# Kernel tuning notes

Measured on AMD Instinct MI355X. Metric: run time of the kernel, lower is better.

Reference implementation:

```python
import jax, jax.numpy as jnp
import numpy as np

EMBED_DIM = 512
NUM_HEADS = 8
HEAD_DIM = EMBED_DIM // NUM_HEADS
FACTOR = 5
B, T = 4, 2048


def setup_inputs() -> dict:
    key = jax.random.key(0)
    ks = jax.random.split(key, 10)
    s = EMBED_DIM ** -0.5
    hidden_states = jax.random.normal(ks[0], (B, T, EMBED_DIM), dtype=jnp.float32)
    log_L = int(np.ceil(np.log1p(T)))
    u_part = min(FACTOR * T * log_L, T)
    index_sample = jax.random.randint(ks[1], (u_part,), 0, T, dtype=jnp.int32)
    Wq = jax.random.normal(ks[2], (EMBED_DIM, EMBED_DIM), dtype=jnp.float32) * s
    bq = jnp.zeros((EMBED_DIM,), dtype=jnp.float32)
    Wk = jax.random.normal(ks[3], (EMBED_DIM, EMBED_DIM), dtype=jnp.float32) * s
    bk = jnp.zeros((EMBED_DIM,), dtype=jnp.float32)
    Wv = jax.random.normal(ks[4], (EMBED_DIM, EMBED_DIM), dtype=jnp.float32) * s
    bv = jnp.zeros((EMBED_DIM,), dtype=jnp.float32)
    Wo = jax.random.normal(ks[5], (EMBED_DIM, EMBED_DIM), dtype=jnp.float32) * s
    bo = jnp.zeros((EMBED_DIM,), dtype=jnp.float32)
    return {"hidden_states": hidden_states, "index_sample": index_sample,
            "Wq": Wq, "bq": bq, "Wk": Wk, "bk": bk, "Wv": Wv, "bv": bv,
            "Wo": Wo, "bo": bo}


def _split_heads(x, bsz, seqlen):
    # [B, T, E] -> [B*H, T, head_dim]
    return x.reshape(bsz, seqlen, NUM_HEADS, HEAD_DIM).transpose(0, 2, 1, 3).reshape(bsz * NUM_HEADS, seqlen, HEAD_DIM)


def reference(hidden_states, index_sample, Wq, bq, Wk, bk, Wv, bv, Wo, bo):
    bsz, tgt_len, embed_dim = hidden_states.shape
    scaling = HEAD_DIM ** -0.5
    q = (hidden_states @ Wq.T + bq) * scaling
    k = hidden_states @ Wk.T + bk
    v = hidden_states @ Wv.T + bv
    q = _split_heads(q, bsz, tgt_len)   # [BH, T, d]
    k = _split_heads(k, bsz, tgt_len)
    v = _split_heads(v, bsz, tgt_len)
    L_k = tgt_len
    log_q = int(np.ceil(np.log1p(tgt_len)))
    u = min(FACTOR * log_q, tgt_len)
    # random key sampling (indices precomputed, length u_part)
    k_sample = k[:, index_sample, :]                                  # [BH, u_part, d]
    qk_sample = jnp.einsum('bqd,bkd->bqk', q, k_sample)               # [BH, T, u_part]
    # sparsity measurement: max - mean over sampled keys (mean uses full L_k as in source)
    sparsity = qk_sample.max(axis=-1) - qk_sample.sum(axis=-1) / L_k  # [BH, T]
    top_idx = jax.lax.top_k(sparsity, u)[1]                           # [BH, u]
    q_reduce = jnp.take_along_axis(q, top_idx[:, :, None], axis=1)    # [BH, u, d]
    attn = jax.nn.softmax(jnp.einsum('bud,bkd->buk', q_reduce, k), axis=-1)  # [BH, u, L]
    attn_out = jnp.einsum('buk,bkd->bud', attn, v)                    # [BH, u, d]
    # encoder context: mean of values over time, scattered with active-query outputs
    context = jnp.broadcast_to(v.mean(axis=1, keepdims=True), v.shape)  # [BH, T, d]
    bh_idx = jnp.arange(bsz * NUM_HEADS)[:, None]
    context = context.at[bh_idx, top_idx].set(attn_out)
    out = context.reshape(bsz, NUM_HEADS, tgt_len, HEAD_DIM).transpose(0, 2, 1, 3).reshape(bsz, tgt_len, embed_dim)
    return out @ Wo.T + bo
```

## Files before the change

kernel.cpp:

```cpp
#include <hip/hip_runtime.h>
#include <hip/hip_bf16.h>
#include <math.h>

#define T_LEN 2048
#define EMB   512
#define NHEAD 8
#define HDIM  64
#define BHEADS 32
#define USEL  40

typedef __bf16 bf16v8 __attribute__((ext_vector_type(8)));
typedef _Float16 f16x8 __attribute__((ext_vector_type(8)));
typedef float f32x4 __attribute__((ext_vector_type(4)));
typedef unsigned short u16;

__device__ __forceinline__ void cvt4_hilo(const float4 f, uint2& ph, uint2& pl)
{
    __hip_bfloat16 h0 = __float2bfloat16(f.x);
    __hip_bfloat16 h1 = __float2bfloat16(f.y);
    __hip_bfloat16 h2 = __float2bfloat16(f.z);
    __hip_bfloat16 h3 = __float2bfloat16(f.w);
    __hip_bfloat16 l0 = __float2bfloat16(f.x - __bfloat162float(h0));
    __hip_bfloat16 l1 = __float2bfloat16(f.y - __bfloat162float(h1));
    __hip_bfloat16 l2 = __float2bfloat16(f.z - __bfloat162float(h2));
// ... 493 lines not shown
        else if (w == 1) { gsrc = kp + 4096;  ldst = KH + 4096; }
        else if (w == 2) { gsrc = kp + 8192;  ldst = KL; }
        else             { gsrc = kp + 12288; ldst = KL + 4096; }
        #pragma unroll
        for (int i = 0; i < 8; ++i)
            __builtin_amdgcn_global_load_lds(
                (const __attribute__((address_space(1))) void*)(gsrc + (size_t)lane * 8 + i * 512),
                (__attribute__((address_space(3))) void*)(ldst + i * 512),
                16, 0, 0);
        __syncthreads();

        #pragma unroll
        for (int j = 0; j < 8; ++j) {
            int rb0 = kq * 1024 + (j * 16 + lm) * 8;
            int rb1 = 4096 + kq * 1024 + (j * 16 + lm) * 8;
            f16x8 bh0 = *(const f16x8*)&KH[rb0];
            f16x8 bl0 = *(const f16x8*)&KL[rb0];
            f16x8 bh1 = *(const f16x8*)&KH[rb1];
            f16x8 bl1 = *(const f16x8*)&KL[rb1];
            f32x4 a0 = {0.f, 0.f, 0.f, 0.f};
            f32x4 a1 = {0.f, 0.f, 0.f, 0.f};
            a0 = __builtin_amdgcn_mfma_f32_16x16x32_f16(qh[0][0], bh0, a0, 0, 0, 0);
            a1 = __builtin_amdgcn_mfma_f32_16x16x32_f16(qh[1][0], bh0, a1, 0, 0, 0);
            a0 = __builtin_amdgcn_mfma_f32_16x16x32_f16(qh[0][0], bl0, a0, 0, 0, 0);
            a1 = __builtin_amdgcn_mfma_f32_16x16x32_f16(qh[1][0], bl0, a1, 0, 0, 0);
            a0 = __builtin_amdgcn_mfma_f32_16x16x32_f16(ql[0][0], bh0, a0, 0, 0, 0);
            a1 = __builtin_amdgcn_mfma_f32_16x16x32_f16(ql[1][0], bh0, a1, 0, 0, 0);
            a0 = __builtin_amdgcn_mfma_f32_16x16x32_f16(qh[0][1], bh1, a0, 0, 0, 0);
            a1 = __builtin_amdgcn_mfma_f32_16x16x32_f16(qh[1][1], bh1, a1, 0, 0, 0);
            a0 = __builtin_amdgcn_mfma_f32_16x16x32_f16(qh[0][1], bl1, a0, 0, 0, 0);
            a1 = __builtin_amdgcn_mfma_f32_16x16x32_f16(qh[1][1], bl1, a1, 0, 0, 0);
            a0 = __builtin_amdgcn_mfma_f32_16x16x32_f16(ql[0][1], bh1, a0, 0, 0, 0);
            a1 = __builtin_amdgcn_mfma_f32_16x16x32_f16(ql[1][1], bh1, a1, 0, 0, 0);
            #pragma unroll
            for (int r = 0; r < 4; ++r) {
                vmax[0][r] = fmaxf(vmax[0][r], a0[r]);
                vmax[1][r] = fmaxf(vmax[1][r], a1[r]);
            }
        }
    }

    #pragma unroll
    for (int i = 0; i < 2; ++i)
        #pragma unroll
        for (int r = 0; r < 4; ++r) {
            float m = vmax[i][r];
            m = fmaxf(m, __shfl_xor(m, 1, 64));
            m = fmaxf(m, __shfl_xor(m, 2, 64));
            m = fmaxf(m, __shfl_xor(m, 4, 64));
            m = fmaxf(m, __shfl_xor(m, 8, 64));
            if (lm == 0) smax[w * 32 + i * 16 + kq * 4 + r] = m;
        }
    __syncthreads();

    if (tid < 128)
        spars[bh * T_LEN + q0 + tid] = smax[tid] - sdotL[tid] * (1.0f / 2048.0f);
}

__global__ __launch_bounds__(256)
void sparsity_scan_fb_kernel(const float* __restrict__ q, const float* __restrict__ k,
                             const float* __restrict__ ksum, const int* __restrict__ klist,
                             const int* __restrict__ ncp, float* __restrict__ spars)
{
    alignas(16) __shared__ u16 KH[256 * 40];
    alignas(16) __shared__ u16 KL[256 * 40];
    __shared__ float ksm[64];
    __shared__ float smax[128];
    __shared__ float sdotL[128];

    const int tid = threadIdx.x;
    const int bh = blockIdx.y;
    const int q0 = blockIdx.x * 128;
    const int w = tid >> 6, lane = tid & 63;
    const int lm = lane & 15, kq = lane >> 4;

    const float* qb = q + ((size_t)bh * T_LEN + q0) * HDIM;
    const float4* kb4 = (const float4*)(k + (size_t)bh * T_LEN * HDIM);
    const int ntiles = (ncp[0] + 127) >> 7;

    if (tid < 64) ksm[tid] = ksum[bh * 64 + tid];

    #pragma unroll
    for (int s = 0; s < 8; ++s) {
        int u = tid + 256 * s;
        int row = u >> 4, c4 = u & 15;
        float4 f = *(const float4*)&qb[row * HDIM + c4 * 4];
        uint2 ph, pl;
        cvt4_hilo_h(f, ph, pl);
        int base = ((c4 >> 3) * 128 + row) * 40 + (c4 & 7) * 4;
        *(uint2*)&KH[base] = ph;
        *(uint2*)&KL[base] = pl;
    }
    __syncthreads();

    f16x8 qh[2][2], ql[2][2];
    #pragma unroll
    for (int i = 0; i < 2; ++i)
        #pragma unroll
        for (int c = 0; c < 2; ++c) {
            int ra = (c * 128 + w * 32 + i * 16 + lm) * 40 + kq * 8;
            qh[i][c] = *(const f16x8*)&KH[ra];
            ql[i][c] = *(const f16x8*)&KL[ra];
        }

    {
        float4 k0a = *(const float4*)&ksm[kq * 8];
        float4 k0b = *(const float4*)&ksm[kq * 8 + 4];
        float4 k1a = *(const float4*)&ksm[32 + kq * 8];
        float4 k1b = *(const float4*)&ksm[32 + kq * 8 + 4];
        float kmv[2][8] = {{k0a.x, k0a.y, k0a.z, k0a.w, k0b.x, k0b.y, k0b.z, k0b.w},
                           {k1a.x, k1a.y, k1a.z, k1a.w, k1b.x, k1b.y, k1b.z, k1b.w}};
        #pragma unroll
        for (int i = 0; i < 2; ++i) {
            float sd = 0.f;
            #pragma unroll
            for (int c = 0; c < 2; ++c)
                #pragma unroll
                for (int e = 0; e < 8; ++e)
                    sd = fmaf((float)qh[i][c][e] + (float)ql[i][c][e], kmv[c][e], sd);
            sd += __shfl_xor(sd, 16, 64);
            sd += __shfl_xor(sd, 32, 64);
            if (kq == 0) sdotL[w * 32 + i * 16 + lm] = sd;
        }
    }

    float vmax[2][4];
    #pragma unroll
    for (int i = 0; i < 2; ++i)
        #pragma unroll
        for (int r = 0; r < 4; ++r) vmax[i][r] = -INFINITY;

    for (int kt = 0; kt < ntiles; ++kt) {
        __syncthreads();
        #pragma unroll
        for (int s = 0; s < 8; ++s) {
            int u = tid + 256 * s;
            int row = u >> 4, c4 = u & 15;
            int krow = klist[kt * 128 + row];
            float4 f = kb4[krow * 16 + c4];
            uint2 ph, pl;
            cvt4_hilo_h(f, ph, pl);
            int base = ((c4 >> 3) * 128 + row) * 40 + (c4 & 7) * 4;
            *(uint2*)&KH[base] = ph;
            *(uint2*)&KL[base] = pl;
        }
        __syncthreads();

        #pragma unroll
        for (int j = 0; j < 8; ++j) {
            int rb0 = (j * 16 + lm) * 40 + kq * 8;
            int rb1 = (128 + j * 16 + lm) * 40 + kq * 8;
            f16x8 bh0 = *(const f16x8*)&KH[rb0];
            f16x8 bl0 = *(const f16x8*)&KL[rb0];
            f16x8 bh1 = *(const f16x8*)&KH[rb1];
            f16x8 bl1 = *(const f16x8*)&KL[rb1];
            f32x4 a0 = {0.f, 0.f, 0.f, 0.f};
            f32x4 a1 = {0.f, 0.f, 0.f, 0.f};
            a0 = __builtin_amdgcn_mfma_f32_16x16x32_f16(qh[0][0], bh0, a0, 0, 0, 0);
            a1 = __builtin_amdgcn_mfma_f32_16x16x32_f16(qh[1][0], bh0, a1, 0, 0, 0);
            a0 = __builtin_amdgcn_mfma_f32_16x16x32_f16(qh[0][0], bl0, a0, 0, 0, 0);
            a1 = __builtin_amdgcn_mfma_f32_16x16x32_f16(qh[1][0], bl0, a1, 0, 0, 0);
            a0 = __builtin_amdgcn_mfma_f32_16x16x32_f16(ql[0][0], bh0, a0, 0, 0, 0);
            a1 = __builtin_amdgcn_mfma_f32_16x16x32_f16(ql[1][0], bh0, a1, 0, 0, 0);
            a0 = __builtin_amdgcn_mfma_f32_16x16x32_f16(qh[0][1], bh1, a0, 0, 0, 0);
            a1 = __builtin_amdgcn_mfma_f32_16x16x32_f16(qh[1][1], bh1, a1, 0, 0, 0);
            a0 = __builtin_amdgcn_mfma_f32_16x16x32_f16(qh[0][1], bl1, a0, 0, 0, 0);
            a1 = __builtin_amdgcn_mfma_f32_16x16x32_f16(qh[1][1], bl1, a1, 0, 0, 0);
            a0 = __builtin_amdgcn_mfma_f32_16x16x32_f16(ql[0][1], bh1, a0, 0, 0, 0);
            a1 = __builtin_amdgcn_mfma_f32_16x16x32_f16(ql[1][1], bh1, a1, 0, 0, 0);
            #pragma unroll
            for (int r = 0; r < 4; ++r) {
                vmax[0][r] = fmaxf(vmax[0][r], a0[r]);
                vmax[1][r] = fmaxf(vmax[1][r], a1[r]);
            }
        }
    }

    #pragma unroll
    for (int i = 0; i < 2; ++i)
        #pragma unroll
        for (int r = 0; r < 4; ++r) {
            float m = vmax[i][r];
            m = fmaxf(m, __shfl_xor(m, 1, 64));
            m = fmaxf(m, __shfl_xor(m, 2, 64));
            m = fmaxf(m, __shfl_xor(m, 4, 64));
            m = fmaxf(m, __shfl_xor(m, 8, 64));
            if (lm == 0) smax[w * 32 + i * 16 + kq * 4 + r] = m;
        }
    __syncthreads();

    if (tid < 128)
        spars[bh * T_LEN + q0 + tid] = smax[tid] - sdotL[tid] * (1.0f / 2048.0f);
}

__global__ __launch_bounds__(256)
void topk_kernel(const float* __restrict__ spars, int* __restrict__ topi)
{
    __shared__ unsigned keys[T_LEN];
    __shared__ int hist[256];
    __shared__ int sfx[257];
    __shared__ int sh_need, sh_bin, nsel, neq, cnt2;
    const int bh = blockIdx.x, tid = threadIdx.x;

    #pragma unroll
    for (int s = 0; s < 8; ++s) {
        int j = tid + 256 * s;
        unsigned u = __float_as_uint(spars[bh * T_LEN + j]);
        keys[j] = (u & 0x80000000u) ? ~u : (u | 0x80000000u);
    }
    if (tid == 0) { sh_need = USEL; nsel = 0; neq = 0; cnt2 = 0; }
    __syncthreads();

    unsigned kpref = 0;
    int shift = 24;
    #pragma unroll
    for (int level = 0; level < 4; ++level) {
        const unsigned hi_mask = (shift == 24) ? 0u : (0xFFFFFFFFu << (shift + 8));
        hist[tid] = 0;
        __syncthreads();
        #pragma unroll
        for (int s = 0; s < 8; ++s) {
            unsigned kk = keys[tid + 256 * s];
            if ((kk & hi_mask) == kpref)
                atomicAdd(&hist[(kk >> shift) & 255], 1);
        }
        __syncthreads();
        sfx[tid] = hist[tid];
        if (tid == 0) sfx[256] = 0;
        __syncthreads();
        for (int off = 1; off < 256; off <<= 1) {
            int v = (tid + off < 256) ? sfx[tid + off] : 0;
            __syncthreads();
            sfx[tid] += v;
            __syncthreads();
        }
        const int need = sh_need;
        const int A = (tid == 255) ? 0 : sfx[tid + 1];
        const int here = sfx[tid];
        __syncthreads();
        if (A < need && here >= need) {
            sh_bin = tid;
            sh_need = need - A;
        }
        __syncthreads();
        kpref |= (unsigned)sh_bin << shift;
        shift -= 8;
    }

    const unsigned K = kpref;
    const int need_eq = sh_need;

    #pragma unroll
    for (int s = 0; s < 8; ++s) {
        int j = tid + 256 * s;
        unsigned kk = keys[j];
        if (kk > K) {
            int pos = atomicAdd(&nsel, 1);
            if (pos < USEL) topi[bh * USEL + pos] = j;
        } else if (kk == K) {
            atomicAdd(&neq, 1);
        }
    }
    __syncthreads();
    const int base = nsel;
    const int E = neq;
    __syncthreads();

    if (E == need_eq) {
        #pragma unroll
        for (int s = 0; s < 8; ++s) {
            int j = tid + 256 * s;
            if (keys[j] == K) {
                int pos = atomicAdd(&cnt2, 1);
                if (base + pos < USEL) topi[bh * USEL + base + pos] = j;
            }
        }
    } else {
        #pragma unroll
        for (int s = 0; s < 8; ++s) {
            int j = tid + 256 * s;
            if (keys[j] == K) {
                int rank = 0;
                for (int j2 = 0; j2 < j; ++j2) rank += (keys[j2] == K);
                if (rank < need_eq && base + rank < USEL)
                    topi[bh * USEL + base + rank] = j;
            }
        }
    }
}

__global__ __launch_bounds__(256)
void gather_q_kernel(const float* __restrict__ q, const int* __restrict__ topi,
                     float* __restrict__ qsel)
{
    const int bh = blockIdx.x, tid = threadIdx.x;
    for (int i = tid; i < USEL * HDIM; i += 256) {
        int u = i >> 6, d = i & 63;
        int t = topi[bh * USEL + u] & (T_LEN - 1);
        qsel[(size_t)bh * USEL * HDIM + i] = q[((size_t)bh * T_LEN + t) * HDIM + d];
    }
}

__global__ __launch_bounds__(256)
void sel_scores_kernel(const float* __restrict__ qsel, const float* __restrict__ k,
                       float* __restrict__ S)
{
    __shared__ float qsT[64 * 41];
    __shared__ float ksT[64 * 257];

    const int sl = blockIdx.x, bh = blockIdx.y, tid = threadIdx.x;
    const int t0 = sl * 256;

    for (int i = tid; i < USEL * HDIM; i += 256) {
        int u = i >> 6, d = i & 63;
        qsT[d * 41 + u] = qsel[(size_t)bh * USEL * HDIM + i];
    }
    const float4* k4 = (const float4*)(k + (size_t)bh * T_LEN * HDIM);
    #pragma unroll
    for (int s = 0; s < 16; ++s) {
        int u = tid + 256 * s;
        int c4 = u & 15, t = u >> 4;
        float4 f = k4[(t0 + t) * 16 + c4];
        ksT[(c4 * 4 + 0) * 257 + t] = f.x;
        ksT[(c4 * 4 + 1) * 257 + t] = f.y;
        ksT[(c4 * 4 + 2) * 257 + t] = f.z;
        ksT[(c4 * 4 + 3) * 257 + t] = f.w;
    }
    __syncthreads();

    const int qg = tid >> 5;
    const int kg = tid & 31;

    float acc[5][8];
    #pragma unroll
    for (int i = 0; i < 5; ++i)
        #pragma unroll
        for (int j = 0; j < 8; ++j) acc[i][j] = 0.0f;

    #pragma unroll 4
    for (int d = 0; d < 64; ++d) {
        float qv[5], kv[8];
        #pragma unroll
        for (int i = 0; i < 5; ++i) qv[i] = qsT[d * 41 + qg * 5 + i];
        #pragma unroll
        for (int j = 0; j < 8; ++j) kv[j] = ksT[d * 257 + kg + 32 * j];
        #pragma unroll
        for (int i = 0; i < 5; ++i)
            #pragma unroll
            for (int j = 0; j < 8; ++j)
                acc[i][j] = fmaf(qv[i], kv[j], acc[i][j]);
    }

    #pragma unroll
    for (int i = 0; i < 5; ++i) {
        float* sp = &S[((size_t)bh * USEL + qg * 5 + i) * T_LEN + t0 + kg];
        #pragma unroll
        for (int j = 0; j < 8; ++j) sp[32 * j] = acc[i][j];
    }
}

__global__ __launch_bounds__(256)
void sel_softmax_kernel(float* __restrict__ S)
{
    __shared__ float red[256];
    const int row = blockIdx.x, tid = threadIdx.x;
    float* sr = S + (size_t)row * T_LEN;

    float x[8];
    float m = -INFINITY;
    #pragma unroll
    for (int s = 0; s < 8; ++s) { x[s] = sr[tid + 256 * s]; m = fmaxf(m, x[s]); }
    red[tid] = m;
    __syncthreads();
    for (int s = 128; s > 0; s >>= 1) {
        if (tid < s) red[tid] = fmaxf(red[tid], red[tid + s]);
        __syncthreads();
    }
    m = red[0];
    __syncthreads();

    float sum = 0.f;
    #pragma unroll
    for (int s = 0; s < 8; ++s) { x[s] = __expf(x[s] - m); sum += x[s]; }
    red[tid] = sum;
    __syncthreads();
    for (int s = 128; s > 0; s >>= 1) {
        if (tid < s) red[tid] += red[tid + s];
        __syncthreads();
    }
    float inv = 1.0f / red[0];
    #pragma unroll
    for (int s = 0; s < 8; ++s) sr[tid + 256 * s] = x[s] * inv;
}

__global__ __launch_bounds__(256)
void pv_part_kernel(const float* __restrict__ S, const float* __restrict__ v,
                    float* __restrict__ part)
{
    __shared__ float ps[USEL * 128];
    __shared__ float vs[128 * 69];
    __shared__ float obuf[128 * 20];

    const int sl = blockIdx.x, bh = blockIdx.y, tid = threadIdx.x;
    const int t0 = sl * 128;

    for (int i = tid; i < USEL * 128; i += 256) {
        int q = i >> 7, t = i & 127;
        ps[q * 128 + t] = S[((size_t)bh * USEL + q) * T_LEN + t0 + t];
    }
    const float4* v4 = (const float4*)(v + (size_t)bh * T_LEN * HDIM);
    #pragma unroll
    for (int s = 0; s < 8; ++s) {
        int u = tid + 256 * s;
        int c4 = u & 15, t = u >> 4;
        float4 f = v4[(t0 + t) * 16 + c4];
        vs[t * 69 + c4 * 4 + 0] = f.x;
        vs[t * 69 + c4 * 4 + 1] = f.y;
        vs[t * 69 + c4 * 4 + 2] = f.z;
        vs[t * 69 + c4 * 4 + 3] = f.w;
    }
    __syncthreads();

    const int qg = tid >> 5, r = tid & 31;
    const int dg = r >> 1, th = r & 1;
    const int tb = th * 64;

    float o[5][4];
    #pragma unroll
    for (int i = 0; i < 5; ++i)
        #pragma unroll
        for (int j = 0; j < 4; ++j) o[i][j] = 0.0f;

    #pragma unroll 4
    for (int tt = 0; tt < 64; ++tt) {
        int t = tb + tt;
        float pv[5];
        #pragma unroll
        for (int i = 0; i < 5; ++i) pv[i] = ps[(qg * 5 + i) * 128 + t];
        float4 vv = *(const float4*)&vs[t * 69 + dg * 4];
        #pragma unroll
        for (int i = 0; i < 5; ++i) {
            o[i][0] = fmaf(pv[i], vv.x, o[i][0]);
            o[i][1] = fmaf(pv[i], vv.y, o[i][1]);
            o[i][2] = fmaf(pv[i], vv.z, o[i][2]);
            o[i][3] = fmaf(pv[i], vv.w, o[i][3]);
        }
    }

    const int p = qg * 16 + dg;
    if (th == 1) {
        #pragma unroll
        for (int i = 0; i < 5; ++i)
            #pragma unroll
            for (int j = 0; j < 4; ++j) obuf[p * 20 + i * 4 + j] = o[i][j];
    }
    __syncthreads();
    if (th == 0) {
        float* pb = part + ((size_t)bh * 16 + sl) * (USEL * HDIM);
        #pragma unroll
        for (int i = 0; i < 5; ++i)
            #pragma unroll
            for (int j = 0; j < 4; ++j)
                pb[(qg * 5 + i) * HDIM + dg * 4 + j] = o[i][j] + obuf[p * 20 + i * 4 + j];
    }
}

__global__ __launch_bounds__(256)
void pv_merge_kernel(const float* __restrict__ part, float* __restrict__ attn)
{
    const int bh = blockIdx.x, tid = threadIdx.x;
    for (int i = tid; i < USEL * HDIM; i += 256) {
        float s = 0.f;
        #pragma unroll
        for (int sl = 0; sl < 16; ++sl)
            s += part[((size_t)bh * 16 + sl) * (USEL * HDIM) + i];
        attn[(size_t)bh * USEL * HDIM + i] = s;
    }
}

__global__ __launch_bounds__(256)
void ctx_fill_pack_kernel(const float* __restrict__ vmean, u16* __restrict__ CXp)
{
    const int tile = blockIdx.x;
    const int tid = threadIdx.x;
    const int mt = tile >> 4, kt = tile & 15;
    const int bh = ((mt >> 4) << 3) | (kt >> 1);
    const int dbase = (kt & 1) * 32;

    uint4 vh[4], vl[4];
    #pragma unroll
    for (int kq = 0; kq < 4; ++kq) {
        unsigned hw[4], lw[4];
        #pragma unroll
        for (int p = 0; p < 4; ++p) {
            u16 h0, l0, h1, l1;
            cvt1_hilo_h(vmean[bh * 64 + dbase + kq * 8 + p * 2],     h0, l0);
            cvt1_hilo_h(vmean[bh * 64 + dbase + kq * 8 + p * 2 + 1], h1, l1);
            hw[p] = (unsigned)h0 | ((unsigned)h1 << 16);
            lw[p] = (unsigned)l0 | ((unsigned)l1 << 16);
        }
        vh[kq] = make_uint4(hw[0], hw[1], hw[2], hw[3]);
        vl[kq] = make_uint4(lw[0], lw[1], lw[2], lw[3]);
    }

    u16* dst = CXp + (size_t)tile * 8192;
    uint4* dh = (uint4*)dst;
    uint4* dl = (uint4*)(dst + 4096);
    #pragma unroll
    for (int s = 0; s < 2; ++s) {
        int u = tid + 256 * s;
        dh[u] = vh[u >> 7];
        dl[u] = vl[u >> 7];
    }
}

__global__ void ctx_scatter_pack_kernel(const float* __restrict__ attn,
                                        const int* __restrict__ topi,
                                        u16* __restrict__ CXp)
{
    const int u = blockIdx.x, bh = blockIdx.y, d = threadIdx.x;
    const int b = bh >> 3, h = bh & 7;
    const int t = topi[bh * USEL + u] & (T_LEN - 1);
    const int m = b * T_LEN + t;
    const int mt = m >> 7, row = m & 127;
    const int e = h * 64 + d;
    const int kt = e >> 5;
    const int c = e & 31, kq = c >> 3, i = c & 7;
    u16 hh, ll;
    cvt1_hilo_h(attn[((size_t)bh * USEL + u) * HDIM + d], hh, ll);
    u16* base = CXp + (size_t)(mt * 16 + kt) * 8192 + kq * 1024 + row * 8 + i;
    base[0]    = hh;
    base[4096] = ll;
}

__global__ __launch_bounds__(256)
void out_mfma_kernel(const u16* __restrict__ CXp, const u16* __restrict__ Wp,
                     const float* __restrict__ bo, float* __restrict__ out)
{
    alignas(16) __shared__ u16 Ah[2][4096];
    alignas(16) __shared__ u16 Al[2][4096];
    alignas(16) __shared__ u16 Bh[2][4096];
    alignas(16) __shared__ u16 Bl[2][4096];

    const int tid = threadIdx.x;
    const int mt = blockIdx.x;
    const int nt = blockIdx.y;
    const int w = tid >> 6, lane = tid & 63;
    const int wm = w & 1, wn = w >> 1;
    const int lm = lane & 15, kq = lane >> 4;

    const u16* Abase = CXp + (size_t)mt * (16 * 8192);
    const u16* Bbase = Wp + (size_t)(3 * 4 + nt) * (16 * 8192);

    f32x4 acc[4][4];
    #pragma unroll
    for (int i = 0; i < 4; ++i)
        #pragma unroll
        for (int j = 0; j < 4; ++j)
            #pragma unroll
            for (int r = 0; r < 4; ++r) acc[i][j][r] = 0.0f;

    auto stage = [&](int kt, int buf) {
        const u16* at = Abase + kt * 8192;
        const u16* bt = Bbase + kt * 8192;
        const u16* gsrc; u16* ldst;
        if (w == 0)      { gsrc = at;        ldst = &Ah[buf][0]; }
        else if (w == 1) { gsrc = at + 4096; ldst = &Al[buf][0]; }
        else if (w == 2) { gsrc = bt;        ldst = &Bh[buf][0]; }
        else             { gsrc = bt + 4096; ldst = &Bl[buf][0]; }
        #pragma unroll
        for (int i = 0; i < 8; ++i)
            __builtin_amdgcn_global_load_lds(
                (const __attribute__((address_space(1))) void*)(gsrc + (size_t)lane * 8 + i * 512),
                (__attribute__((address_space(3))) void*)(ldst + i * 512),
                16, 0, 0);
    };

    stage(0, 0);

    for (int kt = 0; kt < 16; ++kt) {
        const int cur = kt & 1;
        if (kt + 1 < 16) {
            stage(kt + 1, cur ^ 1);
            asm volatile("s_waitcnt vmcnt(8)" ::: "memory");
        } else {
            asm volatile("s_waitcnt vmcnt(0)" ::: "memory");
        }
        __builtin_amdgcn_s_barrier();
        __builtin_amdgcn_sched_barrier(0);

        f16x8 ah[4], al[4], bh[4], bl[4];
        #pragma unroll
        for (int i = 0; i < 4; ++i) {
            int ar = (wm * 64 + i * 16 + lm) * 8 + kq * 1024;
            int br = (wn * 64 + i * 16 + lm) * 8 + kq * 1024;
            ah[i] = *(const f16x8*)&Ah[cur][ar];
            al[i] = *(const f16x8*)&Al[cur][ar];
            bh[i] = *(const f16x8*)&Bh[cur][br];
            bl[i] = *(const f16x8*)&Bl[cur][br];
        }
        #pragma unroll
        for (int i = 0; i < 4; ++i)
            #pragma unroll
            for (int j = 0; j < 4; ++j) {
                acc[i][j] = __builtin_amdgcn_mfma_f32_16x16x32_f16(ah[i], bh[j], acc[i][j], 0, 0, 0);
                acc[i][j] = __builtin_amdgcn_mfma_f32_16x16x32_f16(ah[i], bl[j], acc[i][j], 0, 0, 0);
                acc[i][j] = __builtin_amdgcn_mfma_f32_16x16x32_f16(al[i], bh[j], acc[i][j], 0, 0, 0);
            }
        __builtin_amdgcn_s_barrier();
    }

    #pragma unroll
    for (int j = 0; j < 4; ++j) {
        int ng = nt * 128 + wn * 64 + j * 16 + lm;
        float bias = bo[ng];
        #pragma unroll
        for (int i = 0; i < 4; ++i)
            #pragma unroll
            for (int r = 0; r < 4; ++r) {
                int mg = mt * 128 + wm * 64 + i * 16 + kq * 4 + r;
                out[(size_t)mg * EMB + ng] = acc[i][j][r] + bias;
            }
    }
}

__global__ __launch_bounds__(256)
void ctx_fill_kernel(const float* __restrict__ vmean, float* __restrict__ ctx)
{
    int flat = blockIdx.x * 256 + threadIdx.x;
    int d = flat & 63, h = (flat >> 6) & 7, b = flat >> 20;
    int bh = (b << 3) | h;
    ctx[flat] = vmean[bh * 64 + d];
}

__global__ void ctx_scatter_kernel(const float* __restrict__ attn, const int* __restrict__ topi,
                                   float* __restrict__ ctx)
{
    const int u = blockIdx.x, bh = blockIdx.y, d = threadIdx.x;
    const int b = bh >> 3, h = bh & 7;
    const int t = topi[bh * USEL + u] & (T_LEN - 1);
    ctx[(size_t)(b * T_LEN + t) * EMB + h * 64 + d] =
        attn[((size_t)bh * USEL + u) * HDIM + d];
}

__global__ __launch_bounds__(256)
void out_proj_kernel(const float* __restrict__ A, const float* __restrict__ Wo,
                     const float* __restrict__ bo, float* __restrict__ out)
{
    alignas(16) __shared__ u16 Ah[128 * 40];
    alignas(16) __shared__ u16 Al[128 * 40];
    alignas(16) __shared__ u16 Bh[128 * 40];
    alignas(16) __shared__ u16 Bl[128 * 40];

    const int tid = threadIdx.x;
    const int m0 = blockIdx.x * 128;
    const int n0 = blockIdx.y * 128;
    const int w = tid >> 6, lane = tid & 63;
    const int wm = w & 1, wn = w >> 1;
    const int lm = lane & 15, kq = lane >> 4;

    f32x4 acc[4][4];
    #pragma unroll
    for (int i = 0; i < 4; ++i)
        #pragma unroll
        for (int j = 0; j < 4; ++j)
            #pragma unroll
            for (int r = 0; r < 4; ++r) acc[i][j][r] = 0.0f;

    for (int kc = 0; kc < EMB; kc += 32) {
        __syncthreads();
        #pragma unroll
        for (int s = 0; s < 4; ++s) {
            int u = tid + 256 * s;
            int row = u >> 3, c4 = u & 7;
            float4 fa = *(const float4*)&A[(size_t)(m0 + row) * EMB + kc + c4 * 4];
            float4 fb = *(const float4*)&Wo[(n0 + row) * EMB + kc + c4 * 4];
            uint2 ph, pl;
            cvt4_hilo(fa, ph, pl);
            *(uint2*)&Ah[row * 40 + c4 * 4] = ph;
            *(uint2*)&Al[row * 40 + c4 * 4] = pl;
            cvt4_hilo(fb, ph, pl);
            *(uint2*)&Bh[row * 40 + c4 * 4] = ph;
            *(uint2*)&Bl[row * 40 + c4 * 4] = pl;
        }
        __syncthreads();

        bf16v8 ah[4], al[4], bh[4], bl[4];
        #pragma unroll
        for (int i = 0; i < 4; ++i) {
            int ra = (wm * 64 + i * 16 + lm) * 40 + kq * 8;
            ah[i] = *(const bf16v8*)&Ah[ra];
            al[i] = *(const bf16v8*)&Al[ra];
            int rb = (wn * 64 + i * 16 + lm) * 40 + kq * 8;
            bh[i] = *(const bf16v8*)&Bh[rb];
            bl[i] = *(const bf16v8*)&Bl[rb];
        }
        #pragma unroll
        for (int i = 0; i < 4; ++i)
            #pragma unroll
            for (int j = 0; j < 4; ++j) {
                acc[i][j] = __builtin_amdgcn_mfma_f32_16x16x32_bf16(ah[i], bh[j], acc[i][j], 0, 0, 0);
                acc[i][j] = __builtin_amdgcn_mfma_f32_16x16x32_bf16(ah[i], bl[j], acc[i][j], 0, 0, 0);
                acc[i][j] = __builtin_amdgcn_mfma_f32_16x16x32_bf16(al[i], bh[j], acc[i][j], 0, 0, 0);
            }
    }

    #pragma unroll
    for (int j = 0; j < 4; ++j) {
        int ng = n0 + wn * 64 + j * 16 + lm;
        float bias = bo[ng];
        #pragma unroll
        for (int i = 0; i < 4; ++i)
            #pragma unroll
            for (int r = 0; r < 4; ++r) {
                int mg = m0 + wm * 64 + i * 16 + kq * 4 + r;
                out[(size_t)mg * EMB + ng] = acc[i][j][r] + bias;
            }
    }
}

__global__ __launch_bounds__(256)
void ws_diag_kernel(float* __restrict__ out, int n, float mib)
{
    int flat = blockIdx.x * 256 + threadIdx.x;
    if (flat < n) out[flat] = mib;
}

extern "C" void kernel_launch(void* const* d_in, const int* in_sizes, int n_in,
                              void* d_out, int out_size, void* d_ws, size_t ws_size,
                              hipStream_t stream)
{
    const float* X = nullptr; const int* idxs = nullptr;
    const float* Wseen[4] = {nullptr, nullptr, nullptr, nullptr};
    const float* bseen[4] = {nullptr, nullptr, nullptr, nullptr};
    int nw = 0, nb = 0, u_part = 2048;
    for (int i = 0; i < n_in; ++i) {
        int sz = in_sizes[i];
        if (sz == EMB * EMB * 16) { if (!X) X = (const float*)d_in[i]; }
        else if (sz == T_LEN)     { if (!idxs) { idxs = (const int*)d_in[i]; u_part = sz; } }
        else if (sz == EMB * EMB) { if (nw < 4) Wseen[nw++] = (const float*)d_in[i]; }
        else if (sz == EMB)       { if (nb < 4) bseen[nb++] = (const float*)d_in[i]; }
    }
    if (!X || !idxs || nw < 4 || nb < 4) {
        X = (const float*)d_in[0]; idxs = (const int*)d_in[1];
        Wseen[0] = (const float*)d_in[2]; bseen[0] = (const float*)d_in[3];
        Wseen[1] = (const float*)d_in[4]; bseen[1] = (const float*)d_in[5];
        Wseen[2] = (const float*)d_in[6]; bseen[2] = (const float*)d_in[7];
        Wseen[3] = (const float*)d_in[8]; bseen[3] = (const float*)d_in[9];
        u_part = in_sizes[1];
    }
    const float *Wq = Wseen[0], *Wk = Wseen[1], *Wv = Wseen[2], *Wo = Wseen[3];
    const float *bq = bseen[0], *bk = bseen[1], *bv = bseen[2], *bo = bseen[3];

    const size_t NEED      = 50951168ULL;
    const size_t XP_B      = 16777216ULL;
    const size_t WP_B      = 4194304ULL;
    const size_t CXP_B     = 16777216ULL;
    const size_t NEED_BIG  = NEED + XP_B + WP_B + CXP_B;
    if (ws_size < NEED) {
        ws_diag_kernel<<<(out_size + 255) / 256, 256, 0, stream>>>(
            (float*)d_out, out_size, (float)(ws_size >> 20));
        return;
    }

    float* ws    = (float*)d_ws;
    float* qw    = ws;
    float* kw    = qw + 4194304;
    float* vw    = kw + 4194304;
    float* tail  = vw + 4194304;
    float* slotA = tail;
    float* spars = tail + 81920;
    int*   count = (int*)(tail + 147456);
    float* ksum  = tail + 149504;
    float* vmean = tail + 151552;
    int*   topi  = (int*)(tail + 153600);
    float* kpart = tail;
    float* vpart = tail + 16384;
    int*   klist = (int*)(tail + 32768);
    int*   ncp   = (int*)(tail + 34816);
    float* S     = qw;
    float* pvp   = qw + 2621440;
    float* qsel  = slotA;
    float* attn  = slotA;
    float* ctx   = (float*)d_ws;
    u16*   Xp    = (u16*)((char*)d_ws + NEED);
    u16*   Wp    = (u16*)((char*)d_ws + NEED + XP_B);
    u16*   CXp   = (u16*)((char*)d_ws + NEED + XP_B + WP_B);
    u16*   Kp    = Xp;

    const bool big = (ws_size >= NEED_BIG);

    if (big) {
        pack_hilo_kernel<<<1280, 256, 0, stream>>>(X, Wq, Wk, Wv, Wo, Xp, Wp);
        qkv_mfma_kernel<<<dim3(64, 4, 3), 256, 0, stream>>>(Xp, Wp, bq, bk, bv, qw, kw, vw);
    } else {
        qkv_proj_kernel<<<dim3(64, 4, 3), 256, 0, stream>>>(X, Wq, bq, Wk, bk, Wv, bv, qw, kw, vw);
    }
    count_compact_kernel<<<1, 256, 0, stream>>>(idxs, u_part, count, klist, ncp);
    ksum_vmean_part_kernel<<<dim3(8, 32), 256, 0, stream>>>(count, kw, vw, kpart, vpart);
    ksum_vmean_reduce_kernel<<<32, 64, 0, stream>>>(kpart, vpart, ksum, vmean);
    if (big) {
        pack_k_kernel<<<512, 256, 0, stream>>>(kw, klist, ncp, Kp);
        sparsity_scan_kernel<<<512, 256, 0, stream>>>(qw, Kp, ksum, ncp, spars);
    } else {
        sparsity_scan_fb_kernel<<<dim3(16, 32), 256, 0, stream>>>(qw, kw, ksum, klist, ncp, spars);
    }
    topk_kernel<<<32, 256, 0, stream>>>(spars, topi);
    gather_q_kernel<<<32, 256, 0, stream>>>(qw, topi, qsel);
    sel_scores_kernel<<<dim3(8, 32), 256, 0, stream>>>(qsel, kw, S);
    sel_softmax_kernel<<<1280, 256, 0, stream>>>(S);
    pv_part_kernel<<<dim3(16, 32), 256, 0, stream>>>(S, vw, pvp);
    pv_merge_kernel<<<32, 256, 0, stream>>>(pvp, attn);
    if (big) {
        ctx_fill_pack_kernel<<<1024, 256, 0, stream>>>(vmean, CXp);
        ctx_scatter_pack_kernel<<<dim3(USEL, BHEADS), 64, 0, stream>>>(attn, topi, CXp);
        out_mfma_kernel<<<dim3(64, 4), 256, 0, stream>>>(CXp, Wp, bo, (float*)d_out);
    } else {
        ctx_fill_kernel<<<16384, 256, 0, stream>>>(vmean, ctx);
        ctx_scatter_kernel<<<dim3(USEL, BHEADS), 64, 0, stream>>>(attn, topi, ctx);
        out_proj_kernel<<<dim3(64, 4), 256, 0, stream>>>(ctx, Wo, bo, (float*)d_out);
    }
}
```

Before: 274.1 us.

## Fuse Q gather into scores and merge partial-sum reduction into context packing

On the big-workspace path, the selected-query gather is folded into the score kernel, which now reads q rows directly through topi. The pv_merge, ctx_fill_pack and ctx_scatter_pack kernels become a single ctx_build_pack kernel that reduces the 16 PV partials per selected row and writes them into the packed context tile. This removes three launches and the intermediate qsel/attn round trips. In exchange, S and the PV partials move to a new workspace region, which raises the big-path threshold; if the workspace is too small, the slower fallback path runs instead.

```diff
diff --git a/kernel.cpp b/kernel.cpp
--- a/kernel.cpp
+++ b/kernel.cpp
@@ -819,8 +819,8 @@
 }
 
 __global__ __launch_bounds__(256)
-void sel_scores_kernel(const float* __restrict__ qsel, const float* __restrict__ k,
-                       float* __restrict__ S)
+void sel_scores_direct_kernel(const float* __restrict__ q, const float* __restrict__ k,
+                              const int* __restrict__ topi, float* __restrict__ S)
 {
     __shared__ float qsT[64 * 41];
     __shared__ float ksT[64 * 257];
@@ -830,7 +830,8 @@
 
     for (int i = tid; i < USEL * HDIM; i += 256) {
         int u = i >> 6, d = i & 63;
-        qsT[d * 41 + u] = qsel[(size_t)bh * USEL * HDIM + i];
+        int t = topi[bh * USEL + u] & (T_LEN - 1);
+        qsT[d * 41 + u] = q[((size_t)bh * T_LEN + t) * HDIM + d];
     }
     const float4* k4 = (const float4*)(k + (size_t)bh * T_LEN * HDIM);
     #pragma unroll
@@ -877,6 +878,64 @@
 }
 
 __global__ __launch_bounds__(256)
+void sel_scores_kernel(const float* __restrict__ qsel, const float* __restrict__ k,
+                       float* __restrict__ S)
+{
+    __shared__ float qsT[64 * 41];
+    __shared__ float ksT[64 * 257];
+
+    const int sl = blockIdx.x, bh = blockIdx.y, tid = threadIdx.x;
+    const int t0 = sl * 256;
+
+    for (int i = tid; i < USEL * HDIM; i += 256) {
+        int u = i >> 6, d = i & 63;
+        qsT[d * 41 + u] = qsel[(size_t)bh * USEL * HDIM + i];
+    }
+    const float4* k4 = (const float4*)(k + (size_t)bh * T_LEN * HDIM);
+    #pragma unroll
+    for (int s = 0; s < 16; ++s) {
+        int u = tid + 256 * s;
+        int c4 = u & 15, t = u >> 4;
+        float4 f = k4[(t0 + t) * 16 + c4];
+        ksT[(c4 * 4 + 0) * 257 + t] = f.x;
+        ksT[(c4 * 4 + 1) * 257 + t] = f.y;
+        ksT[(c4 * 4 + 2) * 257 + t] = f.z;
+        ksT[(c4 * 4 + 3) * 257 + t] = f.w;
+    }
+    __syncthreads();
+
+    const int qg = tid >> 5;
+    const int kg = tid & 31;
+
+    float acc[5][8];
+    #pragma unroll
+    for (int i = 0; i < 5; ++i)
+        #pragma unroll
+        for (int j = 0; j < 8; ++j) acc[i][j] = 0.0f;
+
+    #pragma unroll 4
+    for (int d = 0; d < 64; ++d) {
+        float qv[5], kv[8];
+        #pragma unroll
+        for (int i = 0; i < 5; ++i) qv[i] = qsT[d * 41 + qg * 5 + i];
+        #pragma unroll
+        for (int j = 0; j < 8; ++j) kv[j] = ksT[d * 257 + kg + 32 * j];
+        #pragma unroll
+        for (int i = 0; i < 5; ++i)
+            #pragma unroll
+            for (int j = 0; j < 8; ++j)
+                acc[i][j] = fmaf(qv[i], kv[j], acc[i][j]);
+    }
+
+    #pragma unroll
+    for (int i = 0; i < 5; ++i) {
+        float* sp = &S[((size_t)bh * USEL + qg * 5 + i) * T_LEN + t0 + kg];
+        #pragma unroll
+        for (int j = 0; j < 8; ++j) sp[32 * j] = acc[i][j];
+    }
+}
+
+__global__ __launch_bounds__(256)
 void sel_softmax_kernel(float* __restrict__ S)
 {
     __shared__ float red[256];
@@ -996,13 +1055,18 @@
 }
 
 __global__ __launch_bounds__(256)
-void ctx_fill_pack_kernel(const float* __restrict__ vmean, u16* __restrict__ CXp)
+void ctx_build_pack_kernel(const float* __restrict__ vmean,
+                           const float* __restrict__ part,
+                           const int* __restrict__ topi,
+                           u16* __restrict__ CXp)
 {
     const int tile = blockIdx.x;
     const int tid = threadIdx.x;
     const int mt = tile >> 4, kt = tile & 15;
-    const int bh = ((mt >> 4) << 3) | (kt >> 1);
+    const int b = mt >> 4, h = kt >> 1;
+    const int bh = (b << 3) | h;
     const int dbase = (kt & 1) * 32;
+    const int ttile = mt & 15;
 
     uint4 vh[4], vl[4];
     #pragma unroll
@@ -1019,7 +1083,6 @@
         vh[kq] = make_uint4(hw[0], hw[1], hw[2], hw[3]);
         vl[kq] = make_uint4(lw[0], lw[1], lw[2], lw[3]);
     }
-
     u16* dst = CXp + (size_t)tile * 8192;
     uint4* dh = (uint4*)dst;
     uint4* dl = (uint4*)(dst + 4096);
@@ -1029,25 +1092,24 @@
         dh[u] = vh[u >> 7];
         dl[u] = vl[u >> 7];
     }
-}
-
-__global__ void ctx_scatter_pack_kernel(const float* __restrict__ attn,
-                                        const int* __restrict__ topi,
-                                        u16* __restrict__ CXp)
-{
-    const int u = blockIdx.x, bh = blockIdx.y, d = threadIdx.x;
-    const int b = bh >> 3, h = bh & 7;
-    const int t = topi[bh * USEL + u] & (T_LEN - 1);
-    const int m = b * T_LEN + t;
-    const int mt = m >> 7, row = m & 127;
-    const int e = h * 64 + d;
-    const int kt = e >> 5;
-    const int c = e & 31, kq = c >> 3, i = c & 7;
-    u16 hh, ll;
-    cvt1_hilo_h(attn[((size_t)bh * USEL + u) * HDIM + d], hh, ll);
-    u16* base = CXp + (size_t)(mt * 16 + kt) * 8192 + kq * 1024 + row * 8 + i;
-    base[0]    = hh;
-    base[4096] = ll;
+    __syncthreads();
+
+    for (int i = tid; i < USEL * 32; i += 256) {
+        int u = i >> 5, c = i & 31;
+        int t = topi[bh * USEL + u] & (T_LEN - 1);
+        if ((t >> 7) != ttile) continue;
+        int row = t & 127;
+        int d = dbase + c;
+        float s = 0.f;
+        #pragma unroll
+        for (int sl = 0; sl < 16; ++sl)
+            s += part[((size_t)bh * 16 + sl) * (USEL * HDIM) + u * 64 + d];
+        u16 hh, ll;
+        cvt1_hilo_h(s, hh, ll);
+        u16* base = dst + (c >> 3) * 1024 + row * 8 + (c & 7);
+        base[0]    = hh;
+        base[4096] = ll;
+    }
 }
 
 __global__ __launch_bounds__(256)
@@ -1273,7 +1335,9 @@
     const size_t XP_B      = 16777216ULL;
     const size_t WP_B      = 4194304ULL;
     const size_t CXP_B     = 16777216ULL;
-    const size_t NEED_BIG  = NEED + XP_B + WP_B + CXP_B;
+    const size_t S_B       = 10485760ULL;
+    const size_t PVP_B     = 5242880ULL;
+    const size_t NEED_BIG  = NEED + XP_B + WP_B + CXP_B + S_B + PVP_B;
     if (ws_size < NEED) {
         ws_diag_kernel<<<(out_size + 255) / 256, 256, 0, stream>>>(
             (float*)d_out, out_size, (float)(ws_size >> 20));
@@ -1295,14 +1359,16 @@
     float* vpart = tail + 16384;
     int*   klist = (int*)(tail + 32768);
     int*   ncp   = (int*)(tail + 34816);
-    float* S     = qw;
-    float* pvp   = qw + 2621440;
+    float* Sfb   = qw;
+    float* pvpfb = qw + 2621440;
     float* qsel  = slotA;
     float* attn  = slotA;
     float* ctx   = (float*)d_ws;
     u16*   Xp    = (u16*)((char*)d_ws + NEED);
     u16*   Wp    = (u16*)((char*)d_ws + NEED + XP_B);
     u16*   CXp   = (u16*)((char*)d_ws + NEED + XP_B + WP_B);
+    float* S2    = (float*)((char*)d_ws + NEED + XP_B + WP_B + CXP_B);
+    float* pvp2  = S2 + 2621440;
     u16*   Kp    = Xp;
 
     const bool big = (ws_size >= NEED_BIG);
@@ -1323,16 +1389,18 @@
         sparsity_scan_fb_kernel<<<dim3(16, 32), 256, 0, stream>>>(qw, kw, ksum, klist, ncp, spars);
     }
     topk_kernel<<<32, 256, 0, stream>>>(spars, topi);
-    gather_q_kernel<<<32, 256, 0, stream>>>(qw, topi, qsel);
-    sel_scores_kernel<<<dim3(8, 32), 256, 0, stream>>>(qsel, kw, S);
-    sel_softmax_kernel<<<1280, 256, 0, stream>>>(S);
-    pv_part_kernel<<<dim3(16, 32), 256, 0, stream>>>(S, vw, pvp);
-    pv_merge_kernel<<<32, 256, 0, stream>>>(pvp, attn);
     if (big) {
-        ctx_fill_pack_kernel<<<1024, 256, 0, stream>>>(vmean, CXp);
-        ctx_scatter_pack_kernel<<<dim3(USEL, BHEADS), 64, 0, stream>>>(attn, topi, CXp);
+        sel_scores_direct_kernel<<<dim3(8, 32), 256, 0, stream>>>(qw, kw, topi, S2);
+        sel_softmax_kernel<<<1280, 256, 0, stream>>>(S2);
+        pv_part_kernel<<<dim3(16, 32), 256, 0, stream>>>(S2, vw, pvp2);
+        ctx_build_pack_kernel<<<1024, 256, 0, stream>>>(vmean, pvp2, topi, CXp);
         out_mfma_kernel<<<dim3(64, 4), 256, 0, stream>>>(CXp, Wp, bo, (float*)d_out);
     } else {
+        gather_q_kernel<<<32, 256, 0, stream>>>(qw, topi, qsel);
+        sel_scores_kernel<<<dim3(8, 32), 256, 0, stream>>>(qsel, kw, Sfb);
+        sel_softmax_kernel<<<1280, 256, 0, stream>>>(Sfb);
+        pv_part_kernel<<<dim3(16, 32), 256, 0, stream>>>(Sfb, vw, pvpfb);
+        pv_merge_kernel<<<32, 256, 0, stream>>>(pvpfb, attn);
         ctx_fill_kernel<<<16384, 256, 0, stream>>>(vmean, ctx);
         ctx_scatter_kernel<<<dim3(USEL, BHEADS), 64, 0, stream>>>(attn, topi, ctx);
         out_proj_kernel<<<dim3(64, 4), 256, 0, stream>>>(ctx, Wo, bo, (float*)d_out);
```

Result: faster. 266.9 us (median of 2 runs) (-2.6%).
